# Optimization experiments

Measured on AMD Instinct MI355X. Metric: run time of the kernel, lower is better.

## Reference

```python
import jax, jax.numpy as jnp
import numpy as np

B, N, HIST, D, E, NH = 1024, 2, 64, 256, 128, 8
HD = D // NH


def _linear_params(key, fan_in, fan_out):
    kw, kb = jax.random.split(key)
    lim = 1.0 / np.sqrt(fan_in)
    W = jax.random.uniform(kw, (fan_in, fan_out), jnp.float32, -lim, lim)
    b = jax.random.uniform(kb, (fan_out,), jnp.float32, -lim, lim)
    return W, b


def setup_inputs() -> dict:
    key = jax.random.key(0)
    ks = jax.random.split(key, 11)
    inp = {
        "node_features": jax.random.normal(ks[0], (B, N, HIST, D), jnp.float32),
        "edge_features": jax.random.normal(ks[1], (B, E), jnp.float32),
    }
    inp["Wq"], inp["bq"] = _linear_params(ks[2], D, D)
    inp["Wk"], inp["bk"] = _linear_params(ks[3], D, D)
    inp["Wv"], inp["bv"] = _linear_params(ks[4], D, D)
    inp["Wo"], inp["bo"] = _linear_params(ks[5], D, D)
    inp["Wbias"], inp["bbias"] = _linear_params(ks[6], E, NH)
    inp["Wgate"], inp["bgate"] = _linear_params(ks[7], E, D)
    inp["Wscale"], inp["bscale"] = _linear_params(ks[8], E, D)
    inp["Wshift"], inp["bshift"] = _linear_params(ks[9], E, D)
    inp["Whead"], inp["bhead"] = _linear_params(ks[10], E, NH)
    return inp


def reference(node_features, edge_features, Wq, bq, Wk, bk, Wv, bv, Wo, bo,
              Wbias, bbias, Wgate, bgate, Wscale, bscale, Wshift, bshift,
              Whead, bhead) -> jnp.ndarray:
    b, n, hist, d = node_features.shape
    s = n * hist  # seq_len (temporal mode)
    x = node_features.reshape(b, s, d)

    Q = x @ Wq + bq
    K = x @ Wk + bk
    V = x @ Wv + bv

    # Edge-conditioned modulation of V (ECC-style gate/scale/shift)
    gate = jax.nn.sigmoid(edge_features @ Wgate + bgate)      # [b, d]
    scale = jnp.tanh(edge_features @ Wscale + bscale)         # [b, d]
    shift = edge_features @ Wshift + bshift                   # [b, d]
    V = (V * (1.0 + scale[:, None, :]) + shift[:, None, :]) * gate[:, None, :]

    # [b, nh, s, hd]
    Q = Q.reshape(b, s, NH, HD).transpose(0, 2, 1, 3)
    K = K.reshape(b, s, NH, HD).transpose(0, 2, 1, 3)
    V = V.reshape(b, s, NH, HD).transpose(0, 2, 1, 3)

    scores = jnp.einsum('bhqd,bhkd->bhqk', Q, K) * (1.0 / np.sqrt(HD))

    edge_bias = edge_features @ Wbias + bbias                 # [b, nh]
    head_scale = jnp.tanh(edge_features @ Whead + bhead)      # [b, nh]
    scores = scores * (1.0 + head_scale[:, :, None, None])

    # attention bias: edge_bias placed at (t, hist+t) and (hist+t, t)
    t = jnp.arange(hist)
    eb = jnp.broadcast_to(edge_bias[:, :, None], (b, NH, hist))
    attention_bias = jnp.zeros((b, NH, s, s), scores.dtype)
    attention_bias = attention_bias.at[:, :, t, hist + t].set(eb)
    attention_bias = attention_bias.at[:, :, hist + t, t].set(eb)

    attn = jax.nn.softmax(scores + attention_bias, axis=-1)   # dropout in eval mode = identity
    out = jnp.einsum('bhqk,bhkd->bhqd', attn, V)
    out = out.transpose(0, 2, 1, 3).reshape(b, n, hist, d)
    out = out[:, :, -1, :]                                    # last timestep per node
    return out @ Wo + bo
```

## Files before the change

kernel.cpp:

```cpp
#include <hip/hip_runtime.h>
#include <cstdint>
#include <cstddef>


typedef short bf16x8 __attribute__((ext_vector_type(8)));
typedef float f32x4 __attribute__((ext_vector_type(4)));

#define MFMA16(A, B, C) __builtin_amdgcn_mfma_f32_16x16x32_bf16((A), (B), (C), 0, 0, 0)

static __device__ __forceinline__ uint16_t f2bf(float f) {
    uint32_t u = __builtin_bit_cast(uint32_t, f);
    u += 0x7FFFu + ((u >> 16) & 1u);
    return (uint16_t)(u >> 16);
}
static __device__ __forceinline__ uint32_t pack2(float a, float b) {
    return (uint32_t)f2bf(a) | ((uint32_t)f2bf(b) << 16);
}

__global__ __launch_bounds__(256) void k_prep(
    const float* __restrict__ Wq, const float* __restrict__ Wv,
    const float* __restrict__ Wo, const float* __restrict__ Wk,
    uint16_t* __restrict__ WqT, uint16_t* __restrict__ WvT,
    uint16_t* __restrict__ WoT, uint16_t* __restrict__ WkB,
    const float* __restrict__ edge,
    const float* __restrict__ Wgate, const float* __restrict__ bgate,
    const float* __restrict__ Wscale, const float* __restrict__ bscale,
    const float* __restrict__ Wshift, const float* __restrict__ bshift,
    const float* __restrict__ Wbias, const float* __restrict__ bbias,
    const float* __restrict__ Whead, const float* __restrict__ bhead,
    float* __restrict__ sp, float* __restrict__ tp, float* __restrict__ ebhs)
{
    __shared__ float smem[64 * 65];
    const int t = threadIdx.x;
    const int bid = blockIdx.x;
    if (bid < 64) {
        const int z = bid >> 4, tr = (bid >> 2) & 3, tc = bid & 3;
        if (z == 3) {
            #pragma unroll
            for (int i = 0; i < 16; i++) {
                int flat = i * 256 + t;
                int lr = flat >> 6, lc = flat & 63;
                WkB[(size_t)(tr * 64 + lr) * 264 + tc * 64 + lc] =
                    f2bf(Wk[(size_t)(tr * 64 + lr) * 256 + tc * 64 + lc]);
            }
            return;
        }
        const float* W = (z == 0) ? Wq : ((z == 1) ? Wv : Wo);
        uint16_t* O = (z == 0) ? WqT : ((z == 1) ? WvT : WoT);
        float (*tile)[65] = (float (*)[65])smem;
        #pragma unroll
        for (int i = 0; i < 16; i++) {
            int flat = i * 256 + t;
            int lr = flat >> 6, lc = flat & 63;
            tile[lr][lc] = W[(size_t)(tr * 64 + lr) * 256 + tc * 64 + lc];
        }
        __syncthreads();
        #pragma unroll
        for (int i = 0; i < 16; i++) {
            int flat = i * 256 + t;
            int orow = flat >> 6, oc = flat & 63;
            O[(size_t)(tc * 64 + orow) * 264 + tr * 64 + oc] = f2bf(tile[oc][orow]);
        }
        return;
    }
    float* eL = smem;
    const int b0 = (bid - 64) * 4;
    for (int idx = t; idx < 512; idx += 256) {
        int bi = idx >> 7, e = idx & 127;
        eL[bi * 128 + e] = edge[(size_t)(b0 + bi) * 128 + e];
    }
    __syncthreads();
    float ag[4] = {0, 0, 0, 0}, asr[4] = {0, 0, 0, 0}, ah[4] = {0, 0, 0, 0};
    for (int e = 0; e < 128; e++) {
        float wg = Wgate[e * 256 + t];
        float wsc = Wscale[e * 256 + t];
        float wsh = Wshift[e * 256 + t];
        #pragma unroll
        for (int bi = 0; bi < 4; bi++) {
            float xv = eL[bi * 128 + e];
            ag[bi] = fmaf(xv, wg, ag[bi]);
            asr[bi] = fmaf(xv, wsc, asr[bi]);
            ah[bi] = fmaf(xv, wsh, ah[bi]);
        }
    }
    float bg = bgate[t], bs = bscale[t], bsh = bshift[t];
    #pragma unroll
    for (int bi = 0; bi < 4; bi++) {
        float g = 1.0f / (1.0f + __expf(-(ag[bi] + bg)));
        float sc = tanhf(asr[bi] + bs);
        float sh = ah[bi] + bsh;
        sp[(size_t)(b0 + bi) * 256 + t] = (1.0f + sc) * g;
        tp[(size_t)(b0 + bi) * 256 + t] = sh * g;
    }
    if (t < 64) {
        int bi = t >> 4, o = t & 15, h = o & 7;
        const float* W = (o < 8) ? Wbias : Whead;
        float a = 0.0f;
        for (int e = 0; e < 128; e++) a = fmaf(eL[bi * 128 + e], W[e * 8 + h], a);
        float val = (o < 8) ? (a + bbias[h]) : tanhf(a + bhead[h]);
        ebhs[(size_t)(b0 + bi) * 16 + o] = val;
    }
}

__global__ __launch_bounds__(256) void k_qu(
    const float* __restrict__ node, const uint16_t* __restrict__ WqT,
    const uint16_t* __restrict__ WkB, const float* __restrict__ bq,
    uint16_t* __restrict__ U)
{
    __shared__ uint16_t xq[16 * 264];
    __shared__ uint16_t QL[16 * 264];
    const int t = threadIdx.x, lane = t & 63, w = t >> 6, c = lane & 15, quad = lane >> 4;
    const int b0 = blockIdx.x * 4;
    #pragma unroll
    for (int i = 0; i < 4; i++) {
        int flat4 = i * 256 + t;
        int row = flat4 >> 6, c4 = flat4 & 63;
        int r = row & 7;
        int bb = b0 + (r >> 1);
        int s = (r & 1) ? 127 : 63;
        const float4 v = *(const float4*)(node + ((size_t)(bb * 128 + s)) * 256 + c4 * 4);
        uint2 pv; pv.x = pack2(v.x, v.y); pv.y = pack2(v.z, v.w);
        *(uint2*)&xq[row * 264 + c4 * 4] = pv;
    }
    __syncthreads();
    f32x4 zero = {0, 0, 0, 0};
    f32x4 acc[4];
    #pragma unroll
    for (int i = 0; i < 4; i++) acc[i] = zero;
    #pragma unroll
    for (int kk = 0; kk < 8; kk++) {
        bf16x8 afr = *(const bf16x8*)&xq[c * 264 + kk * 32 + quad * 8];
        #pragma unroll
        for (int i = 0; i < 4; i++) {
            int nt = w * 4 + i;
            bf16x8 bfr = *(const bf16x8*)&WqT[(size_t)(nt * 16 + c) * 264 + kk * 32 + quad * 8];
            acc[i] = MFMA16(afr, bfr, acc[i]);
        }
    }
    #pragma unroll
    for (int i = 0; i < 4; i++) {
        int nt = w * 4 + i;
        float bqv = bq[nt * 16 + c];
        #pragma unroll
        for (int r = 0; r < 4; r++) {
            QL[(quad * 4 + r) * 264 + nt * 16 + c] = f2bf(acc[i][r] + bqv);
        }
    }
    __syncthreads();
    for (int hh = 0; hh < 8; hh++) {
        bf16x8 bfr = *(const bf16x8*)&QL[c * 264 + hh * 32 + quad * 8];
        #pragma unroll
        for (int i = 0; i < 4; i++) {
            int mt = w * 4 + i;
            bf16x8 afr = *(const bf16x8*)&WkB[(size_t)(mt * 16 + c) * 264 + hh * 32 + quad * 8];
            f32x4 d = MFMA16(afr, bfr, zero);
            if (c < 8) {
                int bb = b0 + (c >> 1);
                int qh = (c & 1) * 8 + hh;
                uint2 pk; pk.x = pack2(d[0], d[1]); pk.y = pack2(d[2], d[3]);
                *(uint2*)&U[((size_t)(bb * 16 + qh)) * 256 + mt * 16 + quad * 4] = pk;
            }
        }
    }
}

__global__ __launch_bounds__(256, 3) void k_main(
    const float* __restrict__ node,
    const uint16_t* __restrict__ U,
    const float* __restrict__ ebhs,
    uint16_t* __restrict__ Y)
{
    __shared__ uint16_t xc[64 * 264];
    __shared__ uint16_t uL[16 * 264];
    __shared__ uint16_t pL[4 * 16 * 72];
    __shared__ float ebhsL[16];
    const int b = blockIdx.x;
    const int t = threadIdx.x, lane = t & 63, w = t >> 6, c = lane & 15, quad = lane >> 4;

    #pragma unroll
    for (int i = 0; i < 2; i++) {
        int flat = i * 256 + t;
        int row = flat >> 5, c16 = flat & 31;
        uint4 v = *(const uint4*)&U[((size_t)b * 16 + row) * 256 + c16 * 8];
        *(uint4*)&uL[row * 264 + c16 * 8] = v;
    }
    if (t < 16) ebhsL[t] = ebhs[(size_t)b * 16 + t];

    float4 R[16];
    #pragma unroll
    for (int i = 0; i < 16; i++) {
        int flat4 = i * 256 + t;
        int row = flat4 >> 6, c4 = flat4 & 63;
        R[i] = *(const float4*)(node + ((size_t)b * 128 + row) * 256 + c4 * 4);
    }
    #pragma unroll
    for (int i = 0; i < 16; i++) {
        int flat4 = i * 256 + t;
        int row = flat4 >> 6, c4 = flat4 & 63;
        uint2 pv; pv.x = pack2(R[i].x, R[i].y); pv.y = pack2(R[i].z, R[i].w);
        int col = (c4 * 4 + ((row >> 3) & 3) * 16) & 255;
        *(uint2*)&xc[row * 264 + col] = pv;
    }
    __syncthreads();

    const int q = c >> 3, h = c & 7;
    const float scaleF = 0.17677669529663687f * (1.0f + ebhsL[8 + h]);
    const float ebv = ebhsL[h];
    f32x4 zero = {0, 0, 0, 0};
    f32x4 yacc[4];
    #pragma unroll
    for (int tt = 0; tt < 4; tt++) yacc[tt] = zero;
    float mrow = -1e30f, lrow = 0.0f;
    uint16_t* pW = &pL[w * 16 * 72];

    #pragma unroll
    for (int ch = 0; ch < 2; ch++) {
        if (ch == 0) {
            #pragma unroll
            for (int i = 0; i < 16; i++) {
                int flat4 = i * 256 + t;
                int row = flat4 >> 6, c4 = flat4 & 63;
                R[i] = *(const float4*)(node + ((size_t)b * 128 + 64 + row) * 256 + c4 * 4);
            }
        }
        f32x4 sacc[4];
        #pragma unroll
        for (int kt = 0; kt < 4; kt++) sacc[kt] = zero;
        #pragma unroll
        for (int kk = 0; kk < 8; kk++) {
            bf16x8 bfr = *(const bf16x8*)&uL[c * 264 + kk * 32 + quad * 8];
            #pragma unroll
            for (int kt = 0; kt < 4; kt++) {
                int arow = kt * 16 + c;
                int sh = ((arow >> 3) & 3) * 16;
                int colA = (kk * 32 + quad * 8 + sh) & 255;
                bf16x8 afr = *(const bf16x8*)&xc[arow * 264 + colA];
                sacc[kt] = MFMA16(afr, bfr, sacc[kt]);
            }
        }
        float v0[4][4];
        float lmax = -1e30f;
        #pragma unroll
        for (int kt = 0; kt < 4; kt++) {
            #pragma unroll
            for (int r = 0; r < 4; r++) {
                int krow = ch * 64 + kt * 16 + quad * 4 + r;
                float x = sacc[kt][r] * scaleF;
                if ((q == 0 && krow == 127) || (q == 1 && krow == 63)) x += ebv;
                v0[kt][r] = x;
                lmax = fmaxf(lmax, x);
            }
        }
        lmax = fmaxf(lmax, __shfl_xor(lmax, 16, 64));
        lmax = fmaxf(lmax, __shfl_xor(lmax, 32, 64));
        float mnew = fmaxf(mrow, lmax);
        float alpha = __expf(mrow - mnew);
        float lsum = 0.0f;
        #pragma unroll
        for (int kt = 0; kt < 4; kt++) {
            uint2 pk;
            float p0 = __expf(v0[kt][0] - mnew);
            float p1 = __expf(v0[kt][1] - mnew);
            float p2 = __expf(v0[kt][2] - mnew);
            float p3 = __expf(v0[kt][3] - mnew);
            lsum += (p0 + p1) + (p2 + p3);
            pk.x = pack2(p0, p1); pk.y = pack2(p2, p3);
            *(uint2*)&pW[c * 72 + kt * 16 + quad * 4] = pk;
        }
        lsum += __shfl_xor(lsum, 16, 64);
        lsum += __shfl_xor(lsum, 32, 64);
        lrow = lrow * alpha + lsum;
        mrow = mnew;
        #pragma unroll
        for (int r = 0; r < 4; r++) {
            float aj = __shfl(alpha, quad * 4 + r, 64);
            #pragma unroll
            for (int tt = 0; tt < 4; tt++) yacc[tt][r] *= aj;
        }
        #pragma unroll
        for (int kk = 0; kk < 2; kk++) {
            bf16x8 afr = *(const bf16x8*)&pW[c * 72 + kk * 32 + quad * 8];
            int kbase = kk * 32 + quad * 8;
            int sh = ((kbase >> 3) & 3) * 16;
            #pragma unroll
            for (int tt = 0; tt < 4; tt++) {
                int n = w * 64 + tt * 16 + c;
                int col = (n + sh) & 255;
                union { bf16x8 v; uint32_t u[4]; } bb;
                #pragma unroll
                for (int jj = 0; jj < 4; jj++) {
                    uint32_t lo = xc[(kbase + 2 * jj) * 264 + col];
                    uint32_t hi = xc[(kbase + 2 * jj + 1) * 264 + col];
                    bb.u[jj] = lo | (hi << 16);
                }
                yacc[tt] = MFMA16(afr, bb.v, yacc[tt]);
            }
        }
        if (ch == 0) {
            __syncthreads();
            #pragma unroll
            for (int i = 0; i < 16; i++) {
                int flat4 = i * 256 + t;
                int row = flat4 >> 6, c4 = flat4 & 63;
                uint2 pv; pv.x = pack2(R[i].x, R[i].y); pv.y = pack2(R[i].z, R[i].w);
                int col = (c4 * 4 + ((row >> 3) & 3) * 16) & 255;
                *(uint2*)&xc[row * 264 + col] = pv;
            }
            __syncthreads();
        }
    }
    float invr = 1.0f / lrow;
    #pragma unroll
    for (int r = 0; r < 4; r++) {
        float invj = __shfl(invr, quad * 4 + r, 64);
        #pragma unroll
        for (int tt = 0; tt < 4; tt++) {
            int n = w * 64 + tt * 16 + c;
            int qh = quad * 4 + r;
            int hq = qh & 7, qq = qh >> 3;
            Y[((size_t)(hq * 2048 + b * 2 + qq)) * 256 + n] = f2bf(yacc[tt][r] * invj);
        }
    }
}

__global__ __launch_bounds__(256) void k_out(
    const uint16_t* __restrict__ Y,
    const uint16_t* __restrict__ WvT, const uint16_t* __restrict__ WoT,
    const float* __restrict__ bv, const float* __restrict__ bo,
    const float* __restrict__ sp, const float* __restrict__ tp,
    float* __restrict__ out)
{
    __shared__ uint16_t yh[2 * 16 * 264];
    __shared__ uint16_t zm[16 * 264];
    const int t = threadIdx.x, lane = t & 63, w = t >> 6, c = lane & 15, quad = lane >> 4;
    const int R0 = blockIdx.x * 16;
    f32x4 zero = {0, 0, 0, 0};
    for (int hp = 0; hp < 4; hp++) {
        __syncthreads();
        #pragma unroll
        for (int i = 0; i < 4; i++) {
            int flat = i * 256 + t;
            int hl = flat >> 9, rem = flat & 511;
            int row = rem >> 5, c16 = rem & 31;
            uint4 v = *(const uint4*)&Y[((size_t)((2 * hp + hl) * 2048 + R0 + row)) * 256 + c16 * 8];
            *(uint4*)&yh[(hl * 16 + row) * 264 + c16 * 8] = v;
        }
        __syncthreads();
        int hl = w >> 1, nt = w & 1;
        int h = 2 * hp + hl;
        f32x4 zacc = zero;
        #pragma unroll
        for (int kk = 0; kk < 8; kk++) {
            bf16x8 afr = *(const bf16x8*)&yh[(hl * 16 + c) * 264 + kk * 32 + quad * 8];
            bf16x8 bfr = *(const bf16x8*)&WvT[(size_t)(h * 32 + nt * 16 + c) * 264 + kk * 32 + quad * 8];
            zacc = MFMA16(afr, bfr, zacc);
        }
        int col = h * 32 + nt * 16 + c;
        float bvv = bv[col];
        #pragma unroll
        for (int r = 0; r < 4; r++) {
            int row = quad * 4 + r;
            int b = (R0 + row) >> 1;
            float z = zacc[r] + bvv;
            zm[row * 264 + col] = f2bf(z * sp[(size_t)b * 256 + col] + tp[(size_t)b * 256 + col]);
        }
    }
    __syncthreads();
    #pragma unroll
    for (int i = 0; i < 4; i++) {
        int nt = w * 4 + i;
        int n = nt * 16 + c;
        f32x4 fa = zero;
        #pragma unroll
        for (int kk = 0; kk < 8; kk++) {
            bf16x8 afr = *(const bf16x8*)&zm[c * 264 + kk * 32 + quad * 8];
            bf16x8 bfr = *(const bf16x8*)&WoT[(size_t)n * 264 + kk * 32 + quad * 8];
            fa = MFMA16(afr, bfr, fa);
        }
        float bov = bo[n];
        #pragma unroll
        for (int r = 0; r < 4; r++) {
            out[(size_t)(R0 + quad * 4 + r) * 256 + n] = fa[r] + bov;
        }
    }
}

extern "C" void kernel_launch(void* const* d_in, const int* in_sizes, int n_in,
                              void* d_out, int out_size, void* d_ws, size_t ws_size,
                              hipStream_t stream) {
    const float* node   = (const float*)d_in[0];
    const float* edge   = (const float*)d_in[1];
    const float* Wq     = (const float*)d_in[2];
    const float* bq     = (const float*)d_in[3];
    const float* Wk     = (const float*)d_in[4];
    const float* Wv     = (const float*)d_in[6];
    const float* bv     = (const float*)d_in[7];
    const float* Wo     = (const float*)d_in[8];
    const float* bo     = (const float*)d_in[9];
    const float* Wbias  = (const float*)d_in[10];
    const float* bbias  = (const float*)d_in[11];
    const float* Wgate  = (const float*)d_in[12];
    const float* bgate  = (const float*)d_in[13];
    const float* Wscale = (const float*)d_in[14];
    const float* bscale = (const float*)d_in[15];
    const float* Wshift = (const float*)d_in[16];
    const float* bshift = (const float*)d_in[17];
    const float* Whead  = (const float*)d_in[18];
    const float* bhead  = (const float*)d_in[19];

    char* ws = (char*)d_ws;
    uint16_t* WqT  = (uint16_t*)(ws + 0);
    uint16_t* WvT  = (uint16_t*)(ws + 135168);
    uint16_t* WoT  = (uint16_t*)(ws + 270336);
    uint16_t* WkB  = (uint16_t*)(ws + 405504);
    float*    spw  = (float*)(ws + 540672);
    float*    tpw  = (float*)(ws + 1589248);
    float*    ebhs = (float*)(ws + 2637824);
    uint16_t* Uw   = (uint16_t*)(ws + 2703360);
    uint16_t* Yw   = (uint16_t*)(ws + 11091968);

    k_prep<<<320, 256, 0, stream>>>(Wq, Wv, Wo, Wk, WqT, WvT, WoT, WkB,
                                    edge, Wgate, bgate, Wscale, bscale, Wshift, bshift,
                                    Wbias, bbias, Whead, bhead, spw, tpw, ebhs);
    k_qu<<<256, 256, 0, stream>>>(node, WqT, WkB, bq, Uw);
    k_main<<<1024, 256, 0, stream>>>(node, Uw, ebhs, Yw);
    k_out<<<128, 256, 0, stream>>>(Yw, WvT, WoT, bv, bo, spw, tpw, (float*)d_out);
}
```

Measured before the change: 290.0 us.

## Fuse attention with output projection and regroup kernels into three launches

Weight transposition becomes its own kernel. The edge-feature gating math is merged with the Q/U precompute into one launch. The attention kernel now handles four batches per block, keeping per-batch softmax state in registers, and then performs the V-projection, modulation and output projection in place. This removes the Y intermediate round trip through global memory and one kernel launch. In exchange it uses many more registers per block (occupancy hint lowered from 3 to 2) and there are only 256 blocks, which limits parallelism on a large GPU.

```diff
diff --git a/kernel.cpp b/kernel.cpp
--- a/kernel.cpp
+++ b/kernel.cpp
@@ -17,100 +17,100 @@
     return (uint32_t)f2bf(a) | ((uint32_t)f2bf(b) << 16);
 }
 
-__global__ __launch_bounds__(256) void k_prep(
+__global__ __launch_bounds__(256) void k_wt(
     const float* __restrict__ Wq, const float* __restrict__ Wv,
     const float* __restrict__ Wo, const float* __restrict__ Wk,
     uint16_t* __restrict__ WqT, uint16_t* __restrict__ WvT,
-    uint16_t* __restrict__ WoT, uint16_t* __restrict__ WkB,
+    uint16_t* __restrict__ WoT, uint16_t* __restrict__ WkB)
+{
+    const int t = threadIdx.x;
+    const int tr = blockIdx.x, tc = blockIdx.y, z = blockIdx.z;
+    if (z == 3) {
+        #pragma unroll
+        for (int i = 0; i < 16; i++) {
+            int flat = i * 256 + t;
+            int lr = flat >> 6, lc = flat & 63;
+            WkB[(size_t)(tr * 64 + lr) * 264 + tc * 64 + lc] =
+                f2bf(Wk[(size_t)(tr * 64 + lr) * 256 + tc * 64 + lc]);
+        }
+        return;
+    }
+    const float* W = (z == 0) ? Wq : ((z == 1) ? Wv : Wo);
+    uint16_t* O = (z == 0) ? WqT : ((z == 1) ? WvT : WoT);
+    __shared__ float tile[64][65];
+    #pragma unroll
+    for (int i = 0; i < 16; i++) {
+        int flat = i * 256 + t;
+        int lr = flat >> 6, lc = flat & 63;
+        tile[lr][lc] = W[(size_t)(tr * 64 + lr) * 256 + tc * 64 + lc];
+    }
+    __syncthreads();
+    #pragma unroll
+    for (int i = 0; i < 16; i++) {
+        int flat = i * 256 + t;
+        int orow = flat >> 6, oc = flat & 63;
+        O[(size_t)(tc * 64 + orow) * 264 + tr * 64 + oc] = f2bf(tile[oc][orow]);
+    }
+}
+
+__global__ __launch_bounds__(256) void k_eq(
     const float* __restrict__ edge,
     const float* __restrict__ Wgate, const float* __restrict__ bgate,
     const float* __restrict__ Wscale, const float* __restrict__ bscale,
     const float* __restrict__ Wshift, const float* __restrict__ bshift,
     const float* __restrict__ Wbias, const float* __restrict__ bbias,
     const float* __restrict__ Whead, const float* __restrict__ bhead,
-    float* __restrict__ sp, float* __restrict__ tp, float* __restrict__ ebhs)
-{
-    __shared__ float smem[64 * 65];
-    const int t = threadIdx.x;
-    const int bid = blockIdx.x;
-    if (bid < 64) {
-        const int z = bid >> 4, tr = (bid >> 2) & 3, tc = bid & 3;
-        if (z == 3) {
-            #pragma unroll
-            for (int i = 0; i < 16; i++) {
-                int flat = i * 256 + t;
-                int lr = flat >> 6, lc = flat & 63;
-                WkB[(size_t)(tr * 64 + lr) * 264 + tc * 64 + lc] =
-                    f2bf(Wk[(size_t)(tr * 64 + lr) * 256 + tc * 64 + lc]);
-            }
-            return;
-        }
-        const float* W = (z == 0) ? Wq : ((z == 1) ? Wv : Wo);
-        uint16_t* O = (z == 0) ? WqT : ((z == 1) ? WvT : WoT);
-        float (*tile)[65] = (float (*)[65])smem;
-        #pragma unroll
-        for (int i = 0; i < 16; i++) {
-            int flat = i * 256 + t;
-            int lr = flat >> 6, lc = flat & 63;
-            tile[lr][lc] = W[(size_t)(tr * 64 + lr) * 256 + tc * 64 + lc];
-        }
-        __syncthreads();
-        #pragma unroll
-        for (int i = 0; i < 16; i++) {
-            int flat = i * 256 + t;
-            int orow = flat >> 6, oc = flat & 63;
-            O[(size_t)(tc * 64 + orow) * 264 + tr * 64 + oc] = f2bf(tile[oc][orow]);
-        }
-        return;
-    }
-    float* eL = smem;
-    const int b0 = (bid - 64) * 4;
-    for (int idx = t; idx < 512; idx += 256) {
-        int bi = idx >> 7, e = idx & 127;
-        eL[bi * 128 + e] = edge[(size_t)(b0 + bi) * 128 + e];
-    }
-    __syncthreads();
-    float ag[4] = {0, 0, 0, 0}, asr[4] = {0, 0, 0, 0}, ah[4] = {0, 0, 0, 0};
-    for (int e = 0; e < 128; e++) {
-        float wg = Wgate[e * 256 + t];
-        float wsc = Wscale[e * 256 + t];
-        float wsh = Wshift[e * 256 + t];
-        #pragma unroll
-        for (int bi = 0; bi < 4; bi++) {
-            float xv = eL[bi * 128 + e];
-            ag[bi] = fmaf(xv, wg, ag[bi]);
-            asr[bi] = fmaf(xv, wsc, asr[bi]);
-            ah[bi] = fmaf(xv, wsh, ah[bi]);
-        }
-    }
-    float bg = bgate[t], bs = bscale[t], bsh = bshift[t];
-    #pragma unroll
-    for (int bi = 0; bi < 4; bi++) {
-        float g = 1.0f / (1.0f + __expf(-(ag[bi] + bg)));
-        float sc = tanhf(asr[bi] + bs);
-        float sh = ah[bi] + bsh;
-        sp[(size_t)(b0 + bi) * 256 + t] = (1.0f + sc) * g;
-        tp[(size_t)(b0 + bi) * 256 + t] = sh * g;
-    }
-    if (t < 64) {
-        int bi = t >> 4, o = t & 15, h = o & 7;
-        const float* W = (o < 8) ? Wbias : Whead;
-        float a = 0.0f;
-        for (int e = 0; e < 128; e++) a = fmaf(eL[bi * 128 + e], W[e * 8 + h], a);
-        float val = (o < 8) ? (a + bbias[h]) : tanhf(a + bhead[h]);
-        ebhs[(size_t)(b0 + bi) * 16 + o] = val;
-    }
-}
-
-__global__ __launch_bounds__(256) void k_qu(
+    float* __restrict__ sp, float* __restrict__ tp, float* __restrict__ ebhs,
     const float* __restrict__ node, const uint16_t* __restrict__ WqT,
     const uint16_t* __restrict__ WkB, const float* __restrict__ bq,
     uint16_t* __restrict__ U)
 {
-    __shared__ uint16_t xq[16 * 264];
-    __shared__ uint16_t QL[16 * 264];
-    const int t = threadIdx.x, lane = t & 63, w = t >> 6, c = lane & 15, quad = lane >> 4;
-    const int b0 = blockIdx.x * 4;
+    __shared__ char smem[2 * 16 * 264 * 2];
+    const int t = threadIdx.x;
+    if (blockIdx.x < 256) {
+        float* eL = (float*)smem;
+        const int b0 = blockIdx.x * 4;
+        for (int idx = t; idx < 512; idx += 256) {
+            int bi = idx >> 7, e = idx & 127;
+            eL[bi * 128 + e] = edge[(size_t)(b0 + bi) * 128 + e];
+        }
+        __syncthreads();
+        float ag[4] = {0, 0, 0, 0}, asr[4] = {0, 0, 0, 0}, ah[4] = {0, 0, 0, 0};
+        for (int e = 0; e < 128; e++) {
+            float wg = Wgate[e * 256 + t];
+            float wsc = Wscale[e * 256 + t];
+            float wsh = Wshift[e * 256 + t];
+            #pragma unroll
+            for (int bi = 0; bi < 4; bi++) {
+                float xv = eL[bi * 128 + e];
+                ag[bi] = fmaf(xv, wg, ag[bi]);
+                asr[bi] = fmaf(xv, wsc, asr[bi]);
+                ah[bi] = fmaf(xv, wsh, ah[bi]);
+            }
+        }
+        float bg = bgate[t], bs = bscale[t], bsh = bshift[t];
+        #pragma unroll
+        for (int bi = 0; bi < 4; bi++) {
+            float g = 1.0f / (1.0f + __expf(-(ag[bi] + bg)));
+            float sc = tanhf(asr[bi] + bs);
+            float sh = ah[bi] + bsh;
+            sp[(size_t)(b0 + bi) * 256 + t] = (1.0f + sc) * g;
+            tp[(size_t)(b0 + bi) * 256 + t] = sh * g;
+        }
+        if (t < 64) {
+            int bi = t >> 4, o = t & 15, h = o & 7;
+            const float* W = (o < 8) ? Wbias : Whead;
+            float a = 0.0f;
+            for (int e = 0; e < 128; e++) a = fmaf(eL[bi * 128 + e], W[e * 8 + h], a);
+            float val = (o < 8) ? (a + bbias[h]) : tanhf(a + bhead[h]);
+            ebhs[(size_t)(b0 + bi) * 16 + o] = val;
+        }
+        return;
+    }
+    uint16_t* xq = (uint16_t*)smem;
+    uint16_t* QL = (uint16_t*)smem + 16 * 264;
+    const int lane = t & 63, w = t >> 6, c = lane & 15, quad = lane >> 4;
+    const int b0 = (blockIdx.x - 256) * 4;
     #pragma unroll
     for (int i = 0; i < 4; i++) {
         int flat4 = i * 256 + t;
@@ -164,39 +164,42 @@
     }
 }
 
-__global__ __launch_bounds__(256, 3) void k_main(
+__global__ __launch_bounds__(256, 2) void k_mo(
     const float* __restrict__ node,
     const uint16_t* __restrict__ U,
     const float* __restrict__ ebhs,
-    uint16_t* __restrict__ Y)
+    const uint16_t* __restrict__ WvT, const uint16_t* __restrict__ WoT,
+    const float* __restrict__ bv, const float* __restrict__ bo,
+    const float* __restrict__ sp, const float* __restrict__ tp,
+    float* __restrict__ out)
 {
     __shared__ uint16_t xc[64 * 264];
-    __shared__ uint16_t uL[16 * 264];
+    __shared__ uint16_t uL[64 * 264];
     __shared__ uint16_t pL[4 * 16 * 72];
-    __shared__ float ebhsL[16];
-    const int b = blockIdx.x;
+    __shared__ float ebhsL[64];
+    const int b0 = blockIdx.x * 4;
     const int t = threadIdx.x, lane = t & 63, w = t >> 6, c = lane & 15, quad = lane >> 4;
 
     #pragma unroll
-    for (int i = 0; i < 2; i++) {
-        int flat = i * 256 + t;
-        int row = flat >> 5, c16 = flat & 31;
-        uint4 v = *(const uint4*)&U[((size_t)b * 16 + row) * 256 + c16 * 8];
+    for (int i = 0; i < 8; i++) {
+        int id = i * 256 + t;
+        int row = id >> 5, c16 = id & 31;
+        uint4 v = *(const uint4*)&U[((size_t)(b0 * 16) + row) * 256 + c16 * 8];
         *(uint4*)&uL[row * 264 + c16 * 8] = v;
     }
-    if (t < 16) ebhsL[t] = ebhs[(size_t)b * 16 + t];
+    if (t < 64) ebhsL[t] = ebhs[(size_t)b0 * 16 + t];
 
     float4 R[16];
     #pragma unroll
     for (int i = 0; i < 16; i++) {
-        int flat4 = i * 256 + t;
-        int row = flat4 >> 6, c4 = flat4 & 63;
-        R[i] = *(const float4*)(node + ((size_t)b * 128 + row) * 256 + c4 * 4);
+        int f4 = i * 256 + t;
+        int row = f4 >> 6, c4 = f4 & 63;
+        R[i] = *(const float4*)(node + ((size_t)(b0)*128 + row) * 256 + c4 * 4);
     }
     #pragma unroll
     for (int i = 0; i < 16; i++) {
-        int flat4 = i * 256 + t;
-        int row = flat4 >> 6, c4 = flat4 & 63;
+        int f4 = i * 256 + t;
+        int row = f4 >> 6, c4 = f4 & 63;
         uint2 pv; pv.x = pack2(R[i].x, R[i].y); pv.y = pack2(R[i].z, R[i].w);
         int col = (c4 * 4 + ((row >> 3) & 3) * 16) & 255;
         *(uint2*)&xc[row * 264 + col] = pv;
@@ -204,31 +207,35 @@
     __syncthreads();
 
     const int q = c >> 3, h = c & 7;
-    const float scaleF = 0.17677669529663687f * (1.0f + ebhsL[8 + h]);
-    const float ebv = ebhsL[h];
     f32x4 zero = {0, 0, 0, 0};
-    f32x4 yacc[4];
-    #pragma unroll
-    for (int tt = 0; tt < 4; tt++) yacc[tt] = zero;
-    float mrow = -1e30f, lrow = 0.0f;
+    f32x4 yacc[4][4];
+    #pragma unroll
+    for (int bi = 0; bi < 4; bi++)
+        #pragma unroll
+        for (int tt = 0; tt < 4; tt++) yacc[bi][tt] = zero;
+    float mrow[4] = {-1e30f, -1e30f, -1e30f, -1e30f};
+    float lrow[4] = {0, 0, 0, 0};
     uint16_t* pW = &pL[w * 16 * 72];
 
-    #pragma unroll
-    for (int ch = 0; ch < 2; ch++) {
-        if (ch == 0) {
+    for (int p = 0; p < 8; p++) {
+        const int bi = p >> 1, ch = p & 1;
+        if (p < 7) {
+            int nbi = (p + 1) >> 1, nch = (p + 1) & 1;
             #pragma unroll
             for (int i = 0; i < 16; i++) {
-                int flat4 = i * 256 + t;
-                int row = flat4 >> 6, c4 = flat4 & 63;
-                R[i] = *(const float4*)(node + ((size_t)b * 128 + 64 + row) * 256 + c4 * 4);
-            }
-        }
+                int f4 = i * 256 + t;
+                int row = f4 >> 6, c4 = f4 & 63;
+                R[i] = *(const float4*)(node + ((size_t)(b0 + nbi) * 128 + nch * 64 + row) * 256 + c4 * 4);
+            }
+        }
+        const float scaleF = 0.17677669529663687f * (1.0f + ebhsL[bi * 16 + 8 + h]);
+        const float ebv = ebhsL[bi * 16 + h];
         f32x4 sacc[4];
         #pragma unroll
         for (int kt = 0; kt < 4; kt++) sacc[kt] = zero;
         #pragma unroll
         for (int kk = 0; kk < 8; kk++) {
-            bf16x8 bfr = *(const bf16x8*)&uL[c * 264 + kk * 32 + quad * 8];
+            bf16x8 bfr = *(const bf16x8*)&uL[(bi * 16 + c) * 264 + kk * 32 + quad * 8];
             #pragma unroll
             for (int kt = 0; kt < 4; kt++) {
                 int arow = kt * 16 + c;
@@ -253,29 +260,28 @@
         }
         lmax = fmaxf(lmax, __shfl_xor(lmax, 16, 64));
         lmax = fmaxf(lmax, __shfl_xor(lmax, 32, 64));
-        float mnew = fmaxf(mrow, lmax);
-        float alpha = __expf(mrow - mnew);
+        float mnew = fmaxf(mrow[bi], lmax);
+        float alpha = __expf(mrow[bi] - mnew);
         float lsum = 0.0f;
         #pragma unroll
         for (int kt = 0; kt < 4; kt++) {
-            uint2 pk;
             float p0 = __expf(v0[kt][0] - mnew);
             float p1 = __expf(v0[kt][1] - mnew);
             float p2 = __expf(v0[kt][2] - mnew);
             float p3 = __expf(v0[kt][3] - mnew);
             lsum += (p0 + p1) + (p2 + p3);
-            pk.x = pack2(p0, p1); pk.y = pack2(p2, p3);
+            uint2 pk; pk.x = pack2(p0, p1); pk.y = pack2(p2, p3);
             *(uint2*)&pW[c * 72 + kt * 16 + quad * 4] = pk;
         }
         lsum += __shfl_xor(lsum, 16, 64);
         lsum += __shfl_xor(lsum, 32, 64);
-        lrow = lrow * alpha + lsum;
-        mrow = mnew;
+        lrow[bi] = lrow[bi] * alpha + lsum;
+        mrow[bi] = mnew;
         #pragma unroll
         for (int r = 0; r < 4; r++) {
             float aj = __shfl(alpha, quad * 4 + r, 64);
             #pragma unroll
-            for (int tt = 0; tt < 4; tt++) yacc[tt][r] *= aj;
+            for (int tt = 0; tt < 4; tt++) yacc[bi][tt][r] *= aj;
         }
         #pragma unroll
         for (int kk = 0; kk < 2; kk++) {
@@ -293,15 +299,15 @@
                     uint32_t hi = xc[(kbase + 2 * jj + 1) * 264 + col];
                     bb.u[jj] = lo | (hi << 16);
                 }
-                yacc[tt] = MFMA16(afr, bb.v, yacc[tt]);
-            }
-        }
-        if (ch == 0) {
+                yacc[bi][tt] = MFMA16(afr, bb.v, yacc[bi][tt]);
+            }
+        }
+        if (p < 7) {
             __syncthreads();
             #pragma unroll
             for (int i = 0; i < 16; i++) {
-                int flat4 = i * 256 + t;
-                int row = flat4 >> 6, c4 = flat4 & 63;
+                int f4 = i * 256 + t;
+                int row = f4 >> 6, c4 = f4 & 63;
                 uint2 pv; pv.x = pack2(R[i].x, R[i].y); pv.y = pack2(R[i].z, R[i].w);
                 int col = (c4 * 4 + ((row >> 3) & 3) * 16) & 255;
                 *(uint2*)&xc[row * 264 + col] = pv;
@@ -309,78 +315,71 @@
             __syncthreads();
         }
     }
-    float invr = 1.0f / lrow;
-    #pragma unroll
-    for (int r = 0; r < 4; r++) {
-        float invj = __shfl(invr, quad * 4 + r, 64);
-        #pragma unroll
-        for (int tt = 0; tt < 4; tt++) {
-            int n = w * 64 + tt * 16 + c;
-            int qh = quad * 4 + r;
-            int hq = qh & 7, qq = qh >> 3;
-            Y[((size_t)(hq * 2048 + b * 2 + qq)) * 256 + n] = f2bf(yacc[tt][r] * invj);
-        }
-    }
-}
-
-__global__ __launch_bounds__(256) void k_out(
-    const uint16_t* __restrict__ Y,
-    const uint16_t* __restrict__ WvT, const uint16_t* __restrict__ WoT,
-    const float* __restrict__ bv, const float* __restrict__ bo,
-    const float* __restrict__ sp, const float* __restrict__ tp,
-    float* __restrict__ out)
-{
-    __shared__ uint16_t yh[2 * 16 * 264];
-    __shared__ uint16_t zm[16 * 264];
-    const int t = threadIdx.x, lane = t & 63, w = t >> 6, c = lane & 15, quad = lane >> 4;
-    const int R0 = blockIdx.x * 16;
-    f32x4 zero = {0, 0, 0, 0};
-    for (int hp = 0; hp < 4; hp++) {
-        __syncthreads();
-        #pragma unroll
-        for (int i = 0; i < 4; i++) {
-            int flat = i * 256 + t;
-            int hl = flat >> 9, rem = flat & 511;
-            int row = rem >> 5, c16 = rem & 31;
-            uint4 v = *(const uint4*)&Y[((size_t)((2 * hp + hl) * 2048 + R0 + row)) * 256 + c16 * 8];
-            *(uint4*)&yh[(hl * 16 + row) * 264 + c16 * 8] = v;
-        }
-        __syncthreads();
-        int hl = w >> 1, nt = w & 1;
-        int h = 2 * hp + hl;
-        f32x4 zacc = zero;
+
+    __syncthreads();
+    uint16_t* yL = uL;
+    #pragma unroll
+    for (int bi = 0; bi < 4; bi++) {
+        float invr = 1.0f / lrow[bi];
+        #pragma unroll
+        for (int r = 0; r < 4; r++) {
+            float invj = __shfl(invr, quad * 4 + r, 64);
+            #pragma unroll
+            for (int tt = 0; tt < 4; tt++) {
+                int n = w * 64 + tt * 16 + c;
+                yL[(bi * 16 + quad * 4 + r) * 264 + n] = f2bf(yacc[bi][tt][r] * invj);
+            }
+        }
+    }
+    __syncthreads();
+    uint16_t* zm = xc;
+    #pragma unroll
+    for (int hi = 0; hi < 2; hi++) {
+        int hh = w * 2 + hi;
+        f32x4 zacc[2];
+        zacc[0] = zero; zacc[1] = zero;
+        int mr = c & 7;
+        int yrow = (mr >> 1) * 16 + (mr & 1) * 8 + hh;
         #pragma unroll
         for (int kk = 0; kk < 8; kk++) {
-            bf16x8 afr = *(const bf16x8*)&yh[(hl * 16 + c) * 264 + kk * 32 + quad * 8];
-            bf16x8 bfr = *(const bf16x8*)&WvT[(size_t)(h * 32 + nt * 16 + c) * 264 + kk * 32 + quad * 8];
-            zacc = MFMA16(afr, bfr, zacc);
-        }
-        int col = h * 32 + nt * 16 + c;
-        float bvv = bv[col];
-        #pragma unroll
-        for (int r = 0; r < 4; r++) {
-            int row = quad * 4 + r;
-            int b = (R0 + row) >> 1;
-            float z = zacc[r] + bvv;
-            zm[row * 264 + col] = f2bf(z * sp[(size_t)b * 256 + col] + tp[(size_t)b * 256 + col]);
+            bf16x8 afr = *(const bf16x8*)&yL[yrow * 264 + kk * 32 + quad * 8];
+            #pragma unroll
+            for (int nt = 0; nt < 2; nt++) {
+                bf16x8 bfr = *(const bf16x8*)&WvT[(size_t)(hh * 32 + nt * 16 + c) * 264 + kk * 32 + quad * 8];
+                zacc[nt] = MFMA16(afr, bfr, zacc[nt]);
+            }
+        }
+        #pragma unroll
+        for (int nt = 0; nt < 2; nt++) {
+            int col = hh * 32 + nt * 16 + c;
+            float bvv = bv[col];
+            #pragma unroll
+            for (int r = 0; r < 4; r++) {
+                int m = quad * 4 + r;
+                if (m < 8) {
+                    int bb = b0 + (m >> 1);
+                    float z = zacc[nt][r] + bvv;
+                    zm[m * 264 + col] = f2bf(z * sp[(size_t)bb * 256 + col] + tp[(size_t)bb * 256 + col]);
+                }
+            }
         }
     }
     __syncthreads();
     #pragma unroll
     for (int i = 0; i < 4; i++) {
-        int nt = w * 4 + i;
-        int n = nt * 16 + c;
+        int n = (w * 4 + i) * 16 + c;
         f32x4 fa = zero;
         #pragma unroll
         for (int kk = 0; kk < 8; kk++) {
-            bf16x8 afr = *(const bf16x8*)&zm[c * 264 + kk * 32 + quad * 8];
+            bf16x8 afr = *(const bf16x8*)&zm[(c & 7) * 264 + kk * 32 + quad * 8];
             bf16x8 bfr = *(const bf16x8*)&WoT[(size_t)n * 264 + kk * 32 + quad * 8];
             fa = MFMA16(afr, bfr, fa);
         }
         float bov = bo[n];
         #pragma unroll
         for (int r = 0; r < 4; r++) {
-            out[(size_t)(R0 + quad * 4 + r) * 256 + n] = fa[r] + bov;
+            int m = quad * 4 + r;
+            if (m < 8) out[(size_t)(b0 * 2 + m) * 256 + n] = fa[r] + bov;
         }
     }
 }
@@ -417,12 +416,11 @@
     float*    tpw  = (float*)(ws + 1589248);
     float*    ebhs = (float*)(ws + 2637824);
     uint16_t* Uw   = (uint16_t*)(ws + 2703360);
-    uint16_t* Yw   = (uint16_t*)(ws + 11091968);
-
-    k_prep<<<320, 256, 0, stream>>>(Wq, Wv, Wo, Wk, WqT, WvT, WoT, WkB,
-                                    edge, Wgate, bgate, Wscale, bscale, Wshift, bshift,
-                                    Wbias, bbias, Whead, bhead, spw, tpw, ebhs);
-    k_qu<<<256, 256, 0, stream>>>(node, WqT, WkB, bq, Uw);
-    k_main<<<1024, 256, 0, stream>>>(node, Uw, ebhs, Yw);
-    k_out<<<128, 256, 0, stream>>>(Yw, WvT, WoT, bv, bo, spw, tpw, (float*)d_out);
-}
+
+    k_wt<<<dim3(4, 4, 4), 256, 0, stream>>>(Wq, Wv, Wo, Wk, WqT, WvT, WoT, WkB);
+    k_eq<<<512, 256, 0, stream>>>(edge, Wgate, bgate, Wscale, bscale, Wshift, bshift,
+                                  Wbias, bbias, Whead, bhead, spw, tpw, ebhs,
+                                  node, WqT, WkB, bq, Uw);
+    k_mo<<<256, 256, 0, stream>>>(node, Uw, ebhs, WvT, WoT, bv, bo, spw, tpw,
+                                  (float*)d_out);
+}
```

After: 309.1 us. 1.07x slower.
